# Optimization experiments

Measured on AMD Instinct MI355X. Metric: run time of the kernel, lower is better.

Reference implementation:

```python
import jax, jax.numpy as jnp
import numpy as np

B, T = 256, 800
D_IN, H, L, V = 128, 512, 2, 128


def setup_inputs() -> dict:
    key = jax.random.key(0)
    ks = jax.random.split(key, 12)
    s = 0.1  # init scale for stability
    return {
        "W_ih0": jax.random.normal(ks[0], (4 * H, D_IN), jnp.float32) * s,
        "W_hh0": jax.random.normal(ks[1], (4 * H, H), jnp.float32) * s,
        "b_ih0": jax.random.normal(ks[2], (4 * H,), jnp.float32) * s,
        "b_hh0": jax.random.normal(ks[3], (4 * H,), jnp.float32) * s,
        "W_ih1": jax.random.normal(ks[4], (4 * H, H), jnp.float32) * s,
        "W_hh1": jax.random.normal(ks[5], (4 * H, H), jnp.float32) * s,
        "b_ih1": jax.random.normal(ks[6], (4 * H,), jnp.float32) * s,
        "b_hh1": jax.random.normal(ks[7], (4 * H,), jnp.float32) * s,
        "W_lin": jax.random.normal(ks[8], (V, H), jnp.float32) * s,
        "b_lin": jax.random.normal(ks[9], (V,), jnp.float32) * s,
        "z": jax.random.randint(ks[10], (B, T), 0, V, jnp.int32),
        "num_frames": jax.random.randint(ks[11], (B,), 100, 800, jnp.int32),
    }


def _lstm_log_prob(layers, W_lin, b_lin, z, num_frames):
    # teacher-forced inputs: step i sees one_hot(z[:, i-1]), zeros at i=0
    oh = jax.nn.one_hot(z[:, :-1], D_IN, dtype=jnp.float32)          # [B, T-1, D]
    inputs = jnp.concatenate([jnp.zeros((B, 1, D_IN), jnp.float32), oh], axis=1)
    inputs = jnp.transpose(inputs, (1, 0, 2))                         # [T, B, D]

    def step(carry, x_t):
        h, c = carry  # each [L, B, H]
        inp = x_t
        hs, cs = [], []
        for l, (Wih, Whh, bih, bhh) in enumerate(layers):
            gates = inp @ Wih.T + h[l] @ Whh.T + bih + bhh            # [B, 4H]
            i, f, g, o = jnp.split(gates, 4, axis=-1)                 # torch gate order i,f,g,o
            c_new = jax.nn.sigmoid(f) * c[l] + jax.nn.sigmoid(i) * jnp.tanh(g)
            h_new = jax.nn.sigmoid(o) * jnp.tanh(c_new)
            hs.append(h_new)
            cs.append(c_new)
            inp = h_new
        logits_t = inp @ W_lin.T + b_lin                              # [B, V]
        return (jnp.stack(hs), jnp.stack(cs)), logits_t

    h0 = jnp.zeros((L, B, H), jnp.float32)
    c0 = jnp.zeros((L, B, H), jnp.float32)
    _, logits = jax.lax.scan(step, (h0, c0), inputs)                  # [T, B, V]
    logits = jnp.transpose(logits, (1, 0, 2))                         # [B, T, V]

    logp = jax.nn.log_softmax(logits, axis=-1)
    nll = -jnp.take_along_axis(logp, z[..., None].astype(jnp.int32), axis=-1)[..., 0]  # [B, T]
    mask = (jnp.arange(T)[None, :] < num_frames[:, None]).astype(nll.dtype)
    return (nll * mask).mean(axis=-1)                                 # [B] (mean over full T, as in torch)


def reference(W_ih0, W_hh0, b_ih0, b_hh0, W_ih1, W_hh1, b_ih1, b_hh1, W_lin, b_lin, z, num_frames):
    layers = [(W_ih0, W_hh0, b_ih0, b_hh0), (W_ih1, W_hh1, b_ih1, b_hh1)]
    return _lstm_log_prob(layers, W_lin, b_lin, z, num_frames)
```

## Files before the change

kernel.cpp:

```cpp
#include <hip/hip_runtime.h>

#define TT 800

typedef __attribute__((ext_vector_type(8))) short bf16x8;
typedef __attribute__((ext_vector_type(4))) float f32x4;
typedef unsigned short u16;
typedef unsigned int u32;
typedef unsigned long long u64;

constexpr int NCW = 128, NWG = 136, RT = 32;
constexpr size_t WL0A_OFF = 0;
constexpr size_t WL0B_OFF = 2097152;
constexpr size_t WL1_OFF  = 2621440;
constexpr size_t WLIN_OFF = 6815744;
constexpr size_t H0_OFF   = 6946816;
constexpr size_t H1_OFF   = 7471104;
constexpr size_t BAR_OFF  = 7995392;
constexpr int HB = 256 * 512;
constexpr int A_ST = 520;
constexpr int G_OFF_B = 33280;
constexpr int P_OFF_B = 49792;
constexpr int LDS_BYTES = 53248;

__device__ __forceinline__ u16 f2b(float x) {
  u32 u = __float_as_uint(x);
  return (u16)((u + 0x7FFFu + ((u >> 16) & 1u)) >> 16);
}
__device__ __forceinline__ float b2f(u16 v) { return __uint_as_float(((u32)v) << 16); }
__device__ __forceinline__ float sigf(float x) { return 1.f / (1.f + __expf(-x)); }
__device__ __forceinline__ float tanh_f(float x) { float e = __expf(2.f * x); return 1.f - 2.f / (e + 1.f); }

__device__ __forceinline__ void bar_lds() {
  asm volatile("s_waitcnt lgkmcnt(0)" ::: "memory");
  __builtin_amdgcn_s_barrier();
}
__device__ __forceinline__ void bar_full() {
  asm volatile("s_waitcnt vmcnt(0) expcnt(0) lgkmcnt(0)" ::: "memory");
  __builtin_amdgcn_s_barrier();
}

__device__ __forceinline__ u64 ld_coh8(const u64* p) {
  return __hip_atomic_load(p, __ATOMIC_RELAXED, __HIP_MEMORY_SCOPE_AGENT);
}
__device__ __forceinline__ void st_coh8(u64* p, u64 v) {
  __hip_atomic_store(p, v, __ATOMIC_RELAXED, __HIP_MEMORY_SCOPE_AGENT);
}
__device__ __forceinline__ void fadd(u32* f) {
  __hip_atomic_fetch_add(f, 1u, __ATOMIC_RELAXED, __HIP_MEMORY_SCOPE_AGENT);
}
__device__ __forceinline__ void fpoll(u32* f, u32 thr) {
  while (__hip_atomic_load(f, __ATOMIC_RELAXED, __HIP_MEMORY_SCOPE_AGENT) < thr)
    __builtin_amdgcn_s_sleep(1);
}
__device__ __forceinline__ void fadd_l(u32* f) {
  __hip_atomic_fetch_add(f, 1u, __ATOMIC_RELAXED, __HIP_MEMORY_SCOPE_WORKGROUP);
}
__device__ __forceinline__ void fpoll_l(u32* f, u32 thr) {
  while (*(volatile u32*)f < thr) {
    __builtin_amdgcn_s_sleep(1);
    asm volatile("buffer_inv" ::: "memory");
  }
}
__device__ __forceinline__ void l1inv() { asm volatile("buffer_inv" ::: "memory"); }

__global__ void prep_kernel(const float* __restrict__ wih0, const float* __restrict__ whh0,
                            const float* __restrict__ wih1, const float* __restrict__ whh1,
                            const float* __restrict__ wlinf,
                            u16* __restrict__ wl0a, u16* __restrict__ wl0b,
                            u16* __restrict__ wl1, u16* __restrict__ wlin) {
  int i = blockIdx.x * 256 + threadIdx.x;
  const int NA = 2048 * 512, NB = 128 * 2048, N1 = 2048 * 1024, N2 = 128 * 512;
  if (i < NA) {
    int col = i >> 9, k = i & 511;
    wl0a[i] = f2b(whh0[col * 512 + k]);
  } else if (i < NA + NB) {
    int j = i - NA, k = j >> 11, col = j & 2047;
    wl0b[j] = f2b(wih0[col * 128 + k]);
  } else if (i < NA + NB + N1) {
    int j = i - NA - NB, col = j >> 10, k = j & 1023;
    float v = (k < 512) ? wih1[col * 512 + k] : whh1[col * 512 + (k - 512)];
    wl1[j] = f2b(v);
  } else if (i < NA + NB + N1 + N2) {
    int j = i - NA - NB - N1, col = j >> 9, k = j & 511;
    wlin[j] = f2b(wlinf[col * 512 + k]);
  }
}

__global__ __launch_bounds__(256, 1) void lstm_kernel(
    const float* __restrict__ bih0, const float* __restrict__ bhh0,
    const float* __restrict__ bih1, const float* __restrict__ bhh1,
    const float* __restrict__ blin,
    const int* __restrict__ z, const int* __restrict__ nfr,
    const u16* __restrict__ wl0a, const u16* __restrict__ wl0b,
    const u16* __restrict__ wl1, const u16* __restrict__ wlin,
    u16* __restrict__ h0buf, u16* __restrict__ h1buf,
    u32* __restrict__ bars, float* __restrict__ out) {
  extern __shared__ char smem[];
  u16* A = (u16*)smem;
  float* Gf = (float*)(smem + G_OFF_B);
  float* Pm = (float*)(smem + P_OFF_B);
  float* Ps = Pm + 256;
  float* Pt = Ps + 256;
  const int wg = blockIdx.x;
  const int w_all = wg >> 3;
  const bool isC = (w_all < 16);
  const int tile = wg & 7;
  const int w = isC ? w_all : 16;
  const int tid = threadIdx.x, lane = tid & 63, wv = tid >> 6;
  const int l15 = lane & 15, l4 = lane >> 4;
  const int row0 = tile * RT;
  u32* F = bars + tile * 32;
  const f32x4 VZ = {0.f, 0.f, 0.f, 0.f};
  const int rC = tid >> 3, u0C = (tid & 7) * 4;
  const int cuL = tid & 31, rgL = tid >> 5;

  float c0s[4] = {0, 0, 0, 0}, c1s[4] = {0, 0, 0, 0};
  float accN = 0.f, nflv = 0.f;
  float bias0c[2], bias1c[2], biasLc[2];
  bf16x8 bq0R[32];
  bf16x8 bq1R[64];
  bf16x8 wlR[32];

  if (isC) {
#pragma unroll
    for (int cb = 0; cb < 2; ++cb) {
      int col = wv * 512 + w * 32 + cb * 16 + l15;
      bias0c[cb] = bih0[col] + bhh0[col];
      bias1c[cb] = bih1[col] + bhh1[col];
      const u16* b0 = wl0a + (size_t)col * 512 + l4 * 8;
#pragma unroll
      for (int kb = 0; kb < 16; ++kb) bq0R[cb * 16 + kb] = *(const bf16x8*)(b0 + kb * 32);
      const u16* b1 = wl1 + (size_t)col * 1024 + l4 * 8;
#pragma unroll
      for (int kb = 0; kb < 32; ++kb) bq1R[cb * 32 + kb] = *(const bf16x8*)(b1 + kb * 32);
    }
  } else {
#pragma unroll
    for (int cb = 0; cb < 2; ++cb) {
      int colV = wv * 32 + cb * 16 + l15;
      biasLc[cb] = blin[colV];
      const u16* bL = wlin + (size_t)colV * 512 + l4 * 8;
#pragma unroll
      for (int kb = 0; kb < 16; ++kb) wlR[cb * 16 + kb] = *(const bf16x8*)(bL + kb * 32);
    }
    if (rgL == 0) nflv = (float)nfr[row0 + cuL];
  }

  u32 xcc;
  asm volatile("s_getreg_b32 %0, hwreg(HW_REG_XCC_ID)" : "=s"(xcc));
  {
    int* hls = (int*)Pm;
    if (tid == 0) {
      u32 bit = 1u << (xcc & 31u);
      __hip_atomic_fetch_or(bars + 256 + tile, bit, __ATOMIC_RELAXED, __HIP_MEMORY_SCOPE_AGENT);
      __hip_atomic_fetch_add(bars + 272, 1u, __ATOMIC_RELAXED, __HIP_MEMORY_SCOPE_AGENT);
      while (__hip_atomic_load(bars + 272, __ATOMIC_RELAXED, __HIP_MEMORY_SCOPE_AGENT) < (u32)NWG)
        __builtin_amdgcn_s_sleep(1);
      u32 m = __hip_atomic_load(bars + 256 + tile, __ATOMIC_RELAXED, __HIP_MEMORY_SCOPE_AGENT);
      hls[0] = (m == bit) ? 1 : 0;
    }
    __syncthreads();
    const_cast<volatile int&>(hls[0]);
  }
  const bool lok = (((volatile int*)Pm)[0] != 0);
  __syncthreads();

  if (isC && w == 0) {
    u64* z0 = (u64*)(h0buf + HB + row0 * 512);
    u64* z1 = (u64*)(h1buf + row0 * 512);
    u64* z2 = (u64*)(h1buf + HB + row0 * 512);
    if (lok) {
      for (int k = tid; k < 2048; k += 256) { z0[k] = 0; z1[k] = 0; z2[k] = 0; }
    } else {
      for (int k = tid; k < 2048; k += 256) { st_coh8(z0 + k, 0); st_coh8(z1 + k, 0); st_coh8(z2 + k, 0); }
    }
  }
  __syncthreads();
  if (tid == 0) { if (lok) fadd_l(F); else fadd(F); }

  auto ldA = [&](int rb, int kb) {
    return *(const bf16x8*)(A + (rb * 16 + l15) * A_ST + kb * 32 + l4 * 8);
  };

#pragma unroll 1
  for (int tau = 0; tau <= TT + 1; ++tau) {
    if (tid == 0) { if (lok) fpoll_l(F, 17u * (u32)(tau + 1)); else fpoll(F, 17u * (u32)(tau + 1)); }
    bar_lds();
    if (lok) l1inv();
    const u16* h0src = h0buf + ((tau + 1) & 1) * HB + row0 * 512;
    const u64* h1s64 = (const u64*)(h1buf + (tau & 1) * HB + row0 * 512);
    const bool l0act = isC && (tau < TT);
    const bool l1act = isC && (tau >= 1 && tau <= TT);

    if (isC) {
      if (tau <= TT) {
        u64 ta[8], tb[8];
        const u64* s64 = (const u64*)h0src;
        if (lok) {
#pragma unroll
          for (int c = 0; c < 8; ++c) {
            int li = c * 256 + tid;
            ta[c] = s64[li * 2]; tb[c] = s64[li * 2 + 1];
          }
        } else {
#pragma unroll
          for (int c = 0; c < 8; ++c) {
            int li = c * 256 + tid;
            ta[c] = ld_coh8(s64 + li * 2); tb[c] = ld_coh8(s64 + li * 2 + 1);
          }
        }
#pragma unroll
        for (int c = 0; c < 8; ++c) {
          int li = c * 256 + tid, row = li >> 6, cc = li & 63;
          u64* d = (u64*)(A + row * A_ST + cc * 8);
          d[0] = ta[c]; d[1] = tb[c];
        }
      }
      u64 ha[4], hb[4];
      if (l1act) {
        if (lok) {
#pragma unroll
          for (int c = 0; c < 4; ++c) {
            int li = c * 256 + tid;
            ha[c] = h1s64[li * 2]; hb[c] = h1s64[li * 2 + 1];
          }
        } else {
#pragma unroll
          for (int c = 0; c < 4; ++c) {
            int li = c * 256 + tid;
            ha[c] = ld_coh8(h1s64 + li * 2); hb[c] = ld_coh8(h1s64 + li * 2 + 1);
          }
        }
      }
      bar_lds();

      f32x4 acc0[2][2] = {{VZ, VZ}, {VZ, VZ}};
      f32x4 acc1[2][2] = {{VZ, VZ}, {VZ, VZ}};
      if (l0act) {
#pragma unroll
        for (int kb = 0; kb < 16; ++kb) {
          bf16x8 a0 = ldA(0, kb), a1 = ldA(1, kb);
#pragma unroll
          for (int cb = 0; cb < 2; ++cb) {
            acc0[0][cb] = __builtin_amdgcn_mfma_f32_16x16x32_bf16(a0, bq0R[cb * 16 + kb], acc0[0][cb], 0, 0, 0);
            acc0[1][cb] = __builtin_amdgcn_mfma_f32_16x16x32_bf16(a1, bq0R[cb * 16 + kb], acc0[1][cb], 0, 0, 0);
          }
        }
      }
      if (l1act) {
#pragma unroll
        for (int kb = 0; kb < 16; ++kb) {
          bf16x8 a0 = ldA(0, kb), a1 = ldA(1, kb);
#pragma unroll
          for (int cb = 0; cb < 2; ++cb) {
            acc1[0][cb] = __builtin_amdgcn_mfma_f32_16x16x32_bf16(a0, bq1R[cb * 32 + kb], acc1[0][cb], 0, 0, 0);
            acc1[1][cb] = __builtin_amdgcn_mfma_f32_16x16x32_bf16(a1, bq1R[cb * 32 + kb], acc1[1][cb], 0, 0, 0);
          }
        }
      }
      if (l0act) {
#pragma unroll
        for (int rb = 0; rb < 2; ++rb)
#pragma unroll
          for (int cb = 0; cb < 2; ++cb)
#pragma unroll
            for (int q = 0; q < 4; ++q)
              Gf[(rb * 16 + l4 * 4 + q) * 129 + wv * 32 + cb * 16 + l15] = acc0[rb][cb][q] + bias0c[cb];
      }
      bar_lds();

      u64 ha2[4], hb2[4];
      if (l1act) {
        if (lok) {
#pragma unroll
          for (int c = 0; c < 4; ++c) {
            int li = (c + 4) * 256 + tid;
            ha2[c] = h1s64[li * 2]; hb2[c] = h1s64[li * 2 + 1];
          }
        } else {
#pragma unroll
          for (int c = 0; c < 4; ++c) {
            int li = (c + 4) * 256 + tid;
            ha2[c] = ld_coh8(h1s64 + li * 2); hb2[c] = ld_coh8(h1s64 + li * 2 + 1);
          }
        }
      }
      if (l0act) {
        float g4[4][4];
#pragma unroll
        for (int g = 0; g < 4; ++g)
#pragma unroll
          for (int j = 0; j < 4; ++j) g4[g][j] = Gf[rC * 129 + g * 32 + u0C + j];
        if (tau >= 1) {
          int zr = z[(row0 + rC) * TT + (tau - 1)];
          const u16* gb = wl0b + (size_t)zr * 2048 + w * 32 + u0C;
#pragma unroll
          for (int g = 0; g < 4; ++g) {
            u64 v = *(const u64*)(gb + g * 512);
#pragma unroll
            for (int j = 0; j < 4; ++j) g4[g][j] += b2f((u16)(v >> (16 * j)));
          }
        }
        u64 pk = 0;
#pragma unroll
        for (int j = 0; j < 4; ++j) {
          float cn = sigf(g4[1][j]) * c0s[j] + sigf(g4[0][j]) * tanh_f(g4[2][j]);
          float hn = sigf(g4[3][j]) * tanh_f(cn);
          c0s[j] = cn;
          pk |= ((u64)f2b(hn)) << (16 * j);
        }
        u16* h0w = h0buf + (tau & 1) * HB + row0 * 512;
        u64* dst = (u64*)(h0w + rC * 512 + w * 32 + u0C);
        if (lok) *dst = pk; else st_coh8(dst, pk);
      }
      if (l1act) {
#pragma unroll
        for (int c = 0; c < 4; ++c) {
          int li = c * 256 + tid, row = li >> 6, cc = li & 63;
          u64* d = (u64*)(A + row * A_ST + cc * 8);
          d[0] = ha[c]; d[1] = hb[c];
        }
#pragma unroll
        for (int c = 0; c < 4; ++c) {
          int li = (c + 4) * 256 + tid, row = li >> 6, cc = li & 63;
          u64* d = (u64*)(A + row * A_ST + cc * 8);
          d[0] = ha2[c]; d[1] = hb2[c];
        }
      }
      bar_lds();

      if (l1act) {
#pragma unroll
        for (int kb = 16; kb < 32; ++kb) {
          bf16x8 a0 = ldA(0, kb - 16), a1 = ldA(1, kb - 16);
#pragma unroll
          for (int cb = 0; cb < 2; ++cb) {
            acc1[0][cb] = __builtin_amdgcn_mfma_f32_16x16x32_bf16(a0, bq1R[cb * 32 + kb], acc1[0][cb], 0, 0, 0);
            acc1[1][cb] = __builtin_amdgcn_mfma_f32_16x16x32_bf16(a1, bq1R[cb * 32 + kb], acc1[1][cb], 0, 0, 0);
          }
        }
#pragma unroll
        for (int rb = 0; rb < 2; ++rb)
#pragma unroll
          for (int cb = 0; cb < 2; ++cb)
#pragma unroll
            for (int q = 0; q < 4; ++q)
              Gf[(rb * 16 + l4 * 4 + q) * 129 + wv * 32 + cb * 16 + l15] = acc1[rb][cb][q] + bias1c[cb];
      }
      bar_lds();

      if (l1act) {
        float g4[4][4];
#pragma unroll
        for (int g = 0; g < 4; ++g)
#pragma unroll
          for (int j = 0; j < 4; ++j) g4[g][j] = Gf[rC * 129 + g * 32 + u0C + j];
        u64 pk = 0;
#pragma unroll
        for (int j = 0; j < 4; ++j) {
          float cn = sigf(g4[1][j]) * c1s[j] + sigf(g4[0][j]) * tanh_f(g4[2][j]);
          float hn = sigf(g4[3][j]) * tanh_f(cn);
          c1s[j] = cn;
          pk |= ((u64)f2b(hn)) << (16 * j);
        }
        u16* h1w = h1buf + ((tau + 1) & 1) * HB + row0 * 512;
        u64* dst = (u64*)(h1w + rC * 512 + w * 32 + u0C);
        if (lok) *dst = pk; else st_coh8(dst, pk);
      }
      bar_full();
      if (tid == 0) { if (lok) fadd_l(F); else fadd(F); }
    } else {
      const bool lgact = (tau >= 2);
      if (lgact) {
        u64 ta[8], tb[8];
        if (lok) {
#pragma unroll
          for (int c = 0; c < 8; ++c) {
            int li = c * 256 + tid;
            ta[c] = h1s64[li * 2]; tb[c] = h1s64[li * 2 + 1];
          }
        } else {
#pragma unroll
          for (int c = 0; c < 8; ++c) {
            int li = c * 256 + tid;
            ta[c] = ld_coh8(h1s64 + li * 2); tb[c] = ld_coh8(h1s64 + li * 2 + 1);
          }
        }
#pragma unroll
        for (int c = 0; c < 8; ++c) {
          int li = c * 256 + tid, row = li >> 6, cc = li & 63;
          u64* d = (u64*)(A + row * A_ST + cc * 8);
          d[0] = ta[c]; d[1] = tb[c];
        }
      }
      bar_lds();
      if (tid == 0) { if (lok) fadd_l(F); else fadd(F); }
      if (lgact) {
        f32x4 accL[2][2] = {{VZ, VZ}, {VZ, VZ}};
#pragma unroll
        for (int kb = 0; kb < 16; ++kb) {
          bf16x8 a0 = ldA(0, kb), a1 = ldA(1, kb);
#pragma unroll
          for (int cb = 0; cb < 2; ++cb) {
            accL[0][cb] = __builtin_amdgcn_mfma_f32_16x16x32_bf16(a0, wlR[cb * 16 + kb], accL[0][cb], 0, 0, 0);
            accL[1][cb] = __builtin_amdgcn_mfma_f32_16x16x32_bf16(a1, wlR[cb * 16 + kb], accL[1][cb], 0, 0, 0);
          }
        }
#pragma unroll
        for (int rb = 0; rb < 2; ++rb)
#pragma unroll
          for (int cb = 0; cb < 2; ++cb)
#pragma unroll
            for (int q = 0; q < 4; ++q)
              Gf[(rb * 16 + l4 * 4 + q) * 129 + wv * 32 + cb * 16 + l15] = accL[rb][cb][q] + biasLc[cb];
      }
      bar_lds();
      if (lgact) {
        int t2 = tau - 2;
        int r = cuL, k = rgL;
        float vloc[16], mloc = -3.4e38f;
#pragma unroll
        for (int j = 0; j < 16; ++j) {
          vloc[j] = Gf[r * 129 + k * 16 + j];
          mloc = fmaxf(mloc, vloc[j]);
        }
        Pm[r * 8 + k] = mloc;
        bar_lds();
        float mrow = Pm[r * 8];
#pragma unroll
        for (int j = 1; j < 8; ++j) mrow = fmaxf(mrow, Pm[r * 8 + j]);
        int zr = z[(row0 + r) * TT + t2];
        float sloc = 0.f, tloc = 0.f;
#pragma unroll
        for (int j = 0; j < 16; ++j) {
          sloc += __expf(vloc[j] - mrow);
          tloc += (k * 16 + j == zr) ? vloc[j] : 0.f;
        }
        Ps[r * 8 + k] = sloc; Pt[r * 8 + k] = tloc;
        bar_lds();
        if (k == 0) {
          float s = 0.f, tv = 0.f;
#pragma unroll
          for (int j = 0; j < 8; ++j) { s += Ps[r * 8 + j]; tv += Pt[r * 8 + j]; }
          if ((float)t2 < nflv) accN += mrow + __logf(s) - tv;
        }
      } else {
        bar_lds(); bar_lds();
      }
    }
  }

  if (!isC && rgL == 0) out[row0 + cuL] = accN * (1.0f / TT);
}

extern "C" void kernel_launch(void* const* d_in, const int* in_sizes, int n_in,
                              void* d_out, int out_size, void* d_ws, size_t ws_size,
                              hipStream_t stream) {
  const float* wih0 = (const float*)d_in[0];
  const float* whh0 = (const float*)d_in[1];
  const float* bih0 = (const float*)d_in[2];
  const float* bhh0 = (const float*)d_in[3];
  const float* wih1 = (const float*)d_in[4];
  const float* whh1 = (const float*)d_in[5];
  const float* bih1 = (const float*)d_in[6];
  const float* bhh1 = (const float*)d_in[7];
  const float* wlinf = (const float*)d_in[8];
  const float* blin = (const float*)d_in[9];
  const int* z = (const int*)d_in[10];
  const int* nfr = (const int*)d_in[11];
  float* out = (float*)d_out;
  char* ws = (char*)d_ws;
  u16* wl0a = (u16*)(ws + WL0A_OFF);
  u16* wl0b = (u16*)(ws + WL0B_OFF);
  u16* wl1 = (u16*)(ws + WL1_OFF);
  u16* wlin = (u16*)(ws + WLIN_OFF);
  u16* h0buf = (u16*)(ws + H0_OFF);
  u16* h1buf = (u16*)(ws + H1_OFF);
  u32* bars = (u32*)(ws + BAR_OFF);

  hipMemsetAsync(ws + BAR_OFF, 0, 2048, stream);
  const int NTOT = 2048 * 512 + 128 * 2048 + 2048 * 1024 + 128 * 512;
  prep_kernel<<<dim3((NTOT + 255) / 256), dim3(256), 0, stream>>>(
      wih0, whh0, wih1, whh1, wlinf, wl0a, wl0b, wl1, wlin);
  lstm_kernel<<<dim3(NWG), dim3(256), LDS_BYTES, stream>>>(
      bih0, bhh0, bih1, bhh1, blin, z, nfr, wl0a, wl0b, wl1, wlin, h0buf, h1buf, bars, out);
}
```

Before: 7.754 ms.

## Stage layer-1 hidden state in separate LDS buffer to remove mid-step barriers

Adds a second LDS A buffer and separate gate scratch areas, so h0 and h1 are both staged up front. Layer-0 and layer-1 MFMAs now run interleaved in one loop over the shared h0 operand, followed by the h1 half. This drops two block barriers and an LDS restage per timestep. It also prefetches the one-hot input-weight row (z for the next step) before the MFMAs, widens loads to 16-byte vectors, and removes the sleep from the local poll loop. LDS use roughly doubles, which needs a raised dynamic shared-memory attribute.

```diff
diff --git a/kernel.cpp b/kernel.cpp
--- a/kernel.cpp
+++ b/kernel.cpp
@@ -4,11 +4,12 @@
 
 typedef __attribute__((ext_vector_type(8))) short bf16x8;
 typedef __attribute__((ext_vector_type(4))) float f32x4;
+typedef __attribute__((ext_vector_type(2))) unsigned long long u64x2;
 typedef unsigned short u16;
 typedef unsigned int u32;
 typedef unsigned long long u64;
 
-constexpr int NCW = 128, NWG = 136, RT = 32;
+constexpr int NWG = 136, RT = 32;
 constexpr size_t WL0A_OFF = 0;
 constexpr size_t WL0B_OFF = 2097152;
 constexpr size_t WL1_OFF  = 2621440;
@@ -18,9 +19,11 @@
 constexpr size_t BAR_OFF  = 7995392;
 constexpr int HB = 256 * 512;
 constexpr int A_ST = 520;
-constexpr int G_OFF_B = 33280;
-constexpr int P_OFF_B = 49792;
-constexpr int LDS_BYTES = 53248;
+constexpr int A2_OFF_B = 33280;
+constexpr int G0_OFF_B = 66560;
+constexpr int G1_OFF_B = 83072;
+constexpr int P_OFF_B  = 99584;
+constexpr int LDS_BYTES = 102656;
 
 __device__ __forceinline__ u16 f2b(float x) {
   u32 u = __float_as_uint(x);
@@ -57,7 +60,6 @@
 }
 __device__ __forceinline__ void fpoll_l(u32* f, u32 thr) {
   while (*(volatile u32*)f < thr) {
-    __builtin_amdgcn_s_sleep(1);
     asm volatile("buffer_inv" ::: "memory");
   }
 }
@@ -96,8 +98,10 @@
     u16* __restrict__ h0buf, u16* __restrict__ h1buf,
     u32* __restrict__ bars, float* __restrict__ out) {
   extern __shared__ char smem[];
-  u16* A = (u16*)smem;
-  float* Gf = (float*)(smem + G_OFF_B);
+  u16* A  = (u16*)smem;
+  u16* A2 = (u16*)(smem + A2_OFF_B);
+  float* Gf0 = (float*)(smem + G0_OFF_B);
+  float* Gf1 = (float*)(smem + G1_OFF_B);
   float* Pm = (float*)(smem + P_OFF_B);
   float* Ps = Pm + 256;
   float* Pt = Ps + 256;
@@ -181,6 +185,11 @@
   auto ldA = [&](int rb, int kb) {
     return *(const bf16x8*)(A + (rb * 16 + l15) * A_ST + kb * 32 + l4 * 8);
   };
+  auto ldA2 = [&](int rb, int kb) {
+    return *(const bf16x8*)(A2 + (rb * 16 + l15) * A_ST + kb * 32 + l4 * 8);
+  };
+
+  int zcur = 0;
 
 #pragma unroll 1
   for (int tau = 0; tau <= TT + 1; ++tau) {
@@ -193,113 +202,121 @@
     const bool l1act = isC && (tau >= 1 && tau <= TT);
 
     if (isC) {
+      u64x2 tv[8], hv[8];
       if (tau <= TT) {
-        u64 ta[8], tb[8];
         const u64* s64 = (const u64*)h0src;
         if (lok) {
 #pragma unroll
+          for (int c = 0; c < 8; ++c) tv[c] = *(const u64x2*)(s64 + (c * 256 + tid) * 2);
+        } else {
+#pragma unroll
           for (int c = 0; c < 8; ++c) {
             int li = c * 256 + tid;
-            ta[c] = s64[li * 2]; tb[c] = s64[li * 2 + 1];
-          }
+            tv[c][0] = ld_coh8(s64 + li * 2); tv[c][1] = ld_coh8(s64 + li * 2 + 1);
+          }
+        }
+      }
+      if (l1act) {
+        if (lok) {
+#pragma unroll
+          for (int c = 0; c < 8; ++c) hv[c] = *(const u64x2*)(h1s64 + (c * 256 + tid) * 2);
         } else {
 #pragma unroll
           for (int c = 0; c < 8; ++c) {
             int li = c * 256 + tid;
-            ta[c] = ld_coh8(s64 + li * 2); tb[c] = ld_coh8(s64 + li * 2 + 1);
-          }
-        }
+            hv[c][0] = ld_coh8(h1s64 + li * 2); hv[c][1] = ld_coh8(h1s64 + li * 2 + 1);
+          }
+        }
+      }
+      if (tau <= TT) {
 #pragma unroll
         for (int c = 0; c < 8; ++c) {
           int li = c * 256 + tid, row = li >> 6, cc = li & 63;
-          u64* d = (u64*)(A + row * A_ST + cc * 8);
-          d[0] = ta[c]; d[1] = tb[c];
-        }
-      }
-      u64 ha[4], hb[4];
+          *(u64x2*)(A + row * A_ST + cc * 8) = tv[c];
+        }
+      }
       if (l1act) {
-        if (lok) {
-#pragma unroll
-          for (int c = 0; c < 4; ++c) {
-            int li = c * 256 + tid;
-            ha[c] = h1s64[li * 2]; hb[c] = h1s64[li * 2 + 1];
-          }
-        } else {
-#pragma unroll
-          for (int c = 0; c < 4; ++c) {
-            int li = c * 256 + tid;
-            ha[c] = ld_coh8(h1s64 + li * 2); hb[c] = ld_coh8(h1s64 + li * 2 + 1);
-          }
+#pragma unroll
+        for (int c = 0; c < 8; ++c) {
+          int li = c * 256 + tid, row = li >> 6, cc = li & 63;
+          *(u64x2*)(A2 + row * A_ST + cc * 8) = hv[c];
         }
       }
       bar_lds();
+
+      u64 gbv[4] = {0, 0, 0, 0};
+      const bool gact = l0act && (tau >= 1);
+      if (gact) {
+        const u16* gb = wl0b + (size_t)zcur * 2048 + w * 32 + u0C;
+#pragma unroll
+        for (int g = 0; g < 4; ++g) gbv[g] = *(const u64*)(gb + g * 512);
+      }
+      if (tau < TT) zcur = z[(row0 + rC) * TT + tau];
 
       f32x4 acc0[2][2] = {{VZ, VZ}, {VZ, VZ}};
       f32x4 acc1[2][2] = {{VZ, VZ}, {VZ, VZ}};
-      if (l0act) {
+      if (l0act || l1act) {
 #pragma unroll
         for (int kb = 0; kb < 16; ++kb) {
           bf16x8 a0 = ldA(0, kb), a1 = ldA(1, kb);
+          if (l0act) {
+#pragma unroll
+            for (int cb = 0; cb < 2; ++cb) {
+              acc0[0][cb] = __builtin_amdgcn_mfma_f32_16x16x32_bf16(a0, bq0R[cb * 16 + kb], acc0[0][cb], 0, 0, 0);
+              acc0[1][cb] = __builtin_amdgcn_mfma_f32_16x16x32_bf16(a1, bq0R[cb * 16 + kb], acc0[1][cb], 0, 0, 0);
+            }
+          }
+          if (l1act) {
+#pragma unroll
+            for (int cb = 0; cb < 2; ++cb) {
+              acc1[0][cb] = __builtin_amdgcn_mfma_f32_16x16x32_bf16(a0, bq1R[cb * 32 + kb], acc1[0][cb], 0, 0, 0);
+              acc1[1][cb] = __builtin_amdgcn_mfma_f32_16x16x32_bf16(a1, bq1R[cb * 32 + kb], acc1[1][cb], 0, 0, 0);
+            }
+          }
+        }
+      }
+      if (l1act) {
+#pragma unroll
+        for (int kb = 0; kb < 16; ++kb) {
+          bf16x8 a0 = ldA2(0, kb), a1 = ldA2(1, kb);
 #pragma unroll
           for (int cb = 0; cb < 2; ++cb) {
-            acc0[0][cb] = __builtin_amdgcn_mfma_f32_16x16x32_bf16(a0, bq0R[cb * 16 + kb], acc0[0][cb], 0, 0, 0);
-            acc0[1][cb] = __builtin_amdgcn_mfma_f32_16x16x32_bf16(a1, bq0R[cb * 16 + kb], acc0[1][cb], 0, 0, 0);
-          }
-        }
+            acc1[0][cb] = __builtin_amdgcn_mfma_f32_16x16x32_bf16(a0, bq1R[cb * 32 + 16 + kb], acc1[0][cb], 0, 0, 0);
+            acc1[1][cb] = __builtin_amdgcn_mfma_f32_16x16x32_bf16(a1, bq1R[cb * 32 + 16 + kb], acc1[1][cb], 0, 0, 0);
+          }
+        }
+      }
+      if (l0act) {
+#pragma unroll
+        for (int rb = 0; rb < 2; ++rb)
+#pragma unroll
+          for (int cb = 0; cb < 2; ++cb)
+#pragma unroll
+            for (int q = 0; q < 4; ++q)
+              Gf0[(rb * 16 + l4 * 4 + q) * 129 + wv * 32 + cb * 16 + l15] = acc0[rb][cb][q] + bias0c[cb];
       }
       if (l1act) {
 #pragma unroll
-        for (int kb = 0; kb < 16; ++kb) {
-          bf16x8 a0 = ldA(0, kb), a1 = ldA(1, kb);
-#pragma unroll
-          for (int cb = 0; cb < 2; ++cb) {
-            acc1[0][cb] = __builtin_amdgcn_mfma_f32_16x16x32_bf16(a0, bq1R[cb * 32 + kb], acc1[0][cb], 0, 0, 0);
-            acc1[1][cb] = __builtin_amdgcn_mfma_f32_16x16x32_bf16(a1, bq1R[cb * 32 + kb], acc1[1][cb], 0, 0, 0);
-          }
-        }
-      }
-      if (l0act) {
-#pragma unroll
         for (int rb = 0; rb < 2; ++rb)
 #pragma unroll
           for (int cb = 0; cb < 2; ++cb)
 #pragma unroll
             for (int q = 0; q < 4; ++q)
-              Gf[(rb * 16 + l4 * 4 + q) * 129 + wv * 32 + cb * 16 + l15] = acc0[rb][cb][q] + bias0c[cb];
+              Gf1[(rb * 16 + l4 * 4 + q) * 129 + wv * 32 + cb * 16 + l15] = acc1[rb][cb][q] + bias1c[cb];
       }
       bar_lds();
 
-      u64 ha2[4], hb2[4];
-      if (l1act) {
-        if (lok) {
-#pragma unroll
-          for (int c = 0; c < 4; ++c) {
-            int li = (c + 4) * 256 + tid;
-            ha2[c] = h1s64[li * 2]; hb2[c] = h1s64[li * 2 + 1];
-          }
-        } else {
-#pragma unroll
-          for (int c = 0; c < 4; ++c) {
-            int li = (c + 4) * 256 + tid;
-            ha2[c] = ld_coh8(h1s64 + li * 2); hb2[c] = ld_coh8(h1s64 + li * 2 + 1);
-          }
-        }
-      }
       if (l0act) {
         float g4[4][4];
 #pragma unroll
         for (int g = 0; g < 4; ++g)
 #pragma unroll
-          for (int j = 0; j < 4; ++j) g4[g][j] = Gf[rC * 129 + g * 32 + u0C + j];
-        if (tau >= 1) {
-          int zr = z[(row0 + rC) * TT + (tau - 1)];
-          const u16* gb = wl0b + (size_t)zr * 2048 + w * 32 + u0C;
-#pragma unroll
-          for (int g = 0; g < 4; ++g) {
-            u64 v = *(const u64*)(gb + g * 512);
-#pragma unroll
-            for (int j = 0; j < 4; ++j) g4[g][j] += b2f((u16)(v >> (16 * j)));
-          }
+          for (int j = 0; j < 4; ++j) g4[g][j] = Gf0[rC * 129 + g * 32 + u0C + j];
+        if (gact) {
+#pragma unroll
+          for (int g = 0; g < 4; ++g)
+#pragma unroll
+            for (int j = 0; j < 4; ++j) g4[g][j] += b2f((u16)(gbv[g] >> (16 * j)));
         }
         u64 pk = 0;
 #pragma unroll
@@ -314,47 +331,11 @@
         if (lok) *dst = pk; else st_coh8(dst, pk);
       }
       if (l1act) {
-#pragma unroll
-        for (int c = 0; c < 4; ++c) {
-          int li = c * 256 + tid, row = li >> 6, cc = li & 63;
-          u64* d = (u64*)(A + row * A_ST + cc * 8);
-          d[0] = ha[c]; d[1] = hb[c];
-        }
-#pragma unroll
-        for (int c = 0; c < 4; ++c) {
-          int li = (c + 4) * 256 + tid, row = li >> 6, cc = li & 63;
-          u64* d = (u64*)(A + row * A_ST + cc * 8);
-          d[0] = ha2[c]; d[1] = hb2[c];
-        }
-      }
-      bar_lds();
-
-      if (l1act) {
-#pragma unroll
-        for (int kb = 16; kb < 32; ++kb) {
-          bf16x8 a0 = ldA(0, kb - 16), a1 = ldA(1, kb - 16);
-#pragma unroll
-          for (int cb = 0; cb < 2; ++cb) {
-            acc1[0][cb] = __builtin_amdgcn_mfma_f32_16x16x32_bf16(a0, bq1R[cb * 32 + kb], acc1[0][cb], 0, 0, 0);
-            acc1[1][cb] = __builtin_amdgcn_mfma_f32_16x16x32_bf16(a1, bq1R[cb * 32 + kb], acc1[1][cb], 0, 0, 0);
-          }
-        }
-#pragma unroll
-        for (int rb = 0; rb < 2; ++rb)
-#pragma unroll
-          for (int cb = 0; cb < 2; ++cb)
-#pragma unroll
-            for (int q = 0; q < 4; ++q)
-              Gf[(rb * 16 + l4 * 4 + q) * 129 + wv * 32 + cb * 16 + l15] = acc1[rb][cb][q] + bias1c[cb];
-      }
-      bar_lds();
-
-      if (l1act) {
         float g4[4][4];
 #pragma unroll
         for (int g = 0; g < 4; ++g)
 #pragma unroll
-          for (int j = 0; j < 4; ++j) g4[g][j] = Gf[rC * 129 + g * 32 + u0C + j];
+          for (int j = 0; j < 4; ++j) g4[g][j] = Gf1[rC * 129 + g * 32 + u0C + j];
         u64 pk = 0;
 #pragma unroll
         for (int j = 0; j < 4; ++j) {
@@ -372,25 +353,21 @@
     } else {
       const bool lgact = (tau >= 2);
       if (lgact) {
-        u64 ta[8], tb[8];
+        u64x2 ta[8];
         if (lok) {
+#pragma unroll
+          for (int c = 0; c < 8; ++c) ta[c] = *(const u64x2*)(h1s64 + (c * 256 + tid) * 2);
+        } else {
 #pragma unroll
           for (int c = 0; c < 8; ++c) {
             int li = c * 256 + tid;
-            ta[c] = h1s64[li * 2]; tb[c] = h1s64[li * 2 + 1];
-          }
-        } else {
-#pragma unroll
-          for (int c = 0; c < 8; ++c) {
-            int li = c * 256 + tid;
-            ta[c] = ld_coh8(h1s64 + li * 2); tb[c] = ld_coh8(h1s64 + li * 2 + 1);
+            ta[c][0] = ld_coh8(h1s64 + li * 2); ta[c][1] = ld_coh8(h1s64 + li * 2 + 1);
           }
         }
 #pragma unroll
         for (int c = 0; c < 8; ++c) {
           int li = c * 256 + tid, row = li >> 6, cc = li & 63;
-          u64* d = (u64*)(A + row * A_ST + cc * 8);
-          d[0] = ta[c]; d[1] = tb[c];
+          *(u64x2*)(A + row * A_ST + cc * 8) = ta[c];
         }
       }
       bar_lds();
@@ -412,7 +389,7 @@
           for (int cb = 0; cb < 2; ++cb)
 #pragma unroll
             for (int q = 0; q < 4; ++q)
-              Gf[(rb * 16 + l4 * 4 + q) * 129 + wv * 32 + cb * 16 + l15] = accL[rb][cb][q] + biasLc[cb];
+              Gf0[(rb * 16 + l4 * 4 + q) * 129 + wv * 32 + cb * 16 + l15] = accL[rb][cb][q] + biasLc[cb];
       }
       bar_lds();
       if (lgact) {
@@ -421,7 +398,7 @@
         float vloc[16], mloc = -3.4e38f;
 #pragma unroll
         for (int j = 0; j < 16; ++j) {
-          vloc[j] = Gf[r * 129 + k * 16 + j];
+          vloc[j] = Gf0[r * 129 + k * 16 + j];
           mloc = fmaxf(mloc, vloc[j]);
         }
         Pm[r * 8 + k] = mloc;
@@ -478,6 +455,13 @@
   u16* h1buf = (u16*)(ws + H1_OFF);
   u32* bars = (u32*)(ws + BAR_OFF);
 
+  static bool attr_set = false;
+  if (!attr_set) {
+    hipFuncSetAttribute(reinterpret_cast<const void*>(lstm_kernel),
+                        hipFuncAttributeMaxDynamicSharedMemorySize, LDS_BYTES);
+    attr_set = true;
+  }
+
   hipMemsetAsync(ws + BAR_OFF, 0, 2048, stream);
   const int NTOT = 2048 * 512 + 128 * 2048 + 2048 * 1024 + 128 * 512;
   prep_kernel<<<dim3((NTOT + 255) / 256), dim3(256), 0, stream>>>(
```

Measured after the change: 9.579 ms. +23.5%, slower.
